# Kernel tuning notes

Hardware: AMD Instinct MI355X
Metric: run time of the kernel (lower is better)

The kernel has to match this reference:

```python
import jax, jax.numpy as jnp
import numpy as np

EPS = 1e-9  # Dice BatchNorm epsilon

def _dice(x, alpha, mm, mv):
    # Keras BN(center=False, scale=False) in inference mode: (x - moving_mean) / sqrt(moving_var + eps)
    p = jax.nn.sigmoid((x - mm) * jax.lax.rsqrt(mv + EPS))
    return x * (p + alpha * (1.0 - p))

def setup_inputs() -> dict:
    key = jax.random.key(0)
    ks = jax.random.split(key, 8)
    B, T, E = 4096, 200, 12
    return {
        "query": jax.random.normal(ks[0], (B, 1, E), jnp.float32),
        "keys": jax.random.normal(ks[1], (B, T, E), jnp.float32),
        "mask": jnp.ones((B, T), dtype=bool),
        "W0": jax.random.normal(ks[2], (48, 80), jnp.float32) * (1.0 / np.sqrt(48)),
        "b0": jnp.zeros((80,), jnp.float32),
        "W1": jax.random.normal(ks[3], (80, 40), jnp.float32) * (1.0 / np.sqrt(80)),
        "b1": jnp.zeros((40,), jnp.float32),
        "alpha0": jax.random.uniform(ks[4], (80,), jnp.float32),
        "alpha1": jax.random.uniform(ks[5], (40,), jnp.float32),
        "mm0": jnp.zeros((80,), jnp.float32),
        "mv0": jnp.ones((80,), jnp.float32),
        "mm1": jnp.zeros((40,), jnp.float32),
        "mv1": jnp.ones((40,), jnp.float32),
        "atten_kernel": jax.random.normal(ks[6], (40, 1), jnp.float32) * (1.0 / np.sqrt(40)),
        "atten_bias": jnp.zeros((1,), jnp.float32),
    }

def reference(query, keys, mask, W0, b0, W1, b1, alpha0, alpha1,
              mm0, mv0, mm1, mv1, atten_kernel, atten_bias):
    B, T, E = keys.shape
    q = jnp.broadcast_to(query, (B, T, E))  # K.repeat_elements(query, T, 1)
    att = jnp.concatenate([q, keys, q - keys, q * keys], axis=-1)  # [B, T, 4E=48]
    h = _dice(jnp.einsum('bti,io->bto', att, W0) + b0, alpha0, mm0, mv0)  # [B,T,80]
    h = _dice(jnp.einsum('bti,io->bto', h, W1) + b1, alpha1, mm1, mv1)    # [B,T,40]
    score = jnp.einsum('bti,io->bto', h, atten_kernel) + atten_bias       # [B,T,1]
    scores = jnp.swapaxes(score, 1, 2)  # [B,1,T]
    # NOTE: original code computes tf.where(mask,...) but overwrites it and
    # matmuls the UNMASKED scores with keys (bug reproduced faithfully).
    return jnp.matmul(scores, keys)  # [B,1,E]
```

## Files before the change

### kernel.cpp

```cpp
#include <hip/hip_runtime.h>
#include <math.h>

#define B_TOT 4096
#define T_LEN 200
#define E_DIM 12
#define LOG2E 1.44269504088896340736f

typedef __attribute__((ext_vector_type(8))) short     bf16x8;
typedef __attribute__((ext_vector_type(4))) float     f32x4;


__device__ inline unsigned short f2bf(float f) {
    union { float f; unsigned u; } x; x.f = f;
    unsigned r = x.u + 0x7FFFu + ((x.u >> 16) & 1u);
    return (unsigned short)(r >> 16);
}

__global__ __launch_bounds__(256) void din_prep(
    const float* __restrict__ W0, const float* __restrict__ b0v,
    const float* __restrict__ W1, const float* __restrict__ b1v,
    const float* __restrict__ a0, const float* __restrict__ a1,
    const float* __restrict__ mm0, const float* __restrict__ mv0,
    const float* __restrict__ mm1, const float* __restrict__ mv1,
    const float* __restrict__ ak, void* __restrict__ wsv)
{
    unsigned char* wsb = (unsigned char*)wsv;
    unsigned short* w0e = (unsigned short*)wsb;
    unsigned short* w1e = (unsigned short*)(wsb + 10240);
    float* d0c = (float*)(wsb + 19456);
    float* d1c = (float*)(wsb + 20736);

    int idx = blockIdx.x * 256 + threadIdx.x;
    if (idx < 5120) {
        int n = idx >> 6, k = idx & 63;
        float v;
        if (k < 12)        v = W0[(12 + k) * 80 + n] - W0[(24 + k) * 80 + n];
        else if (k < 24)   v = W0[(36 + (k - 12)) * 80 + n];
        else if (k < 36)   v = W0[(k - 24) * 80 + n] + W0[(24 + (k - 24)) * 80 + n];
        else if (k == 36)  v = b0v[n];
        else               v = 0.0f;
        w0e[n * 64 + k] = f2bf(v);
    } else if (idx < 9728) {
        int v2 = idx - 5120;
        int n = v2 / 96, k = v2 - n * 96;
        float v = 0.0f;
        if (n < 40) {
            if (k < 80)       v = W1[k * 40 + n];
            else if (k == 80) v = b1v[n];
        }
        w1e[n * 96 + k] = f2bf(v);
    } else if (idx < 10048) {
        int v2 = idx - 9728;
        int o = v2 >> 2, c = v2 & 3;
        float rs = rsqrtf(mv0[o] + 1e-9f) * LOG2E;
        float val = (c == 0) ? -rs : (c == 1) ? mm0[o] * rs : (c == 2) ? a0[o] : 1.0f - a0[o];
        d0c[o * 4 + c] = val;
    } else {
        int v2 = idx - 10048;
        int j = v2 >> 2, c = v2 & 3;
        float val = 0.0f;
        if (j < 40) {
            float rs = rsqrtf(mv1[j] + 1e-9f) * LOG2E;
            val = (c == 0) ? -rs : (c == 1) ? mm1[j] * rs : (c == 2) ? a1[j] * ak[j]
                                                          : (1.0f - a1[j]) * ak[j];
        }
        d1c[j * 4 + c] = val;
    }
}

#define A0_STRIDE 72
#define H_STRIDE  104

__global__ __launch_bounds__(256, 2) void din_mfma(
    const float* __restrict__ query, const float* __restrict__ keys,
    const float* __restrict__ abias_p, const void* __restrict__ wsv,
    float* __restrict__ out)
{
    __shared__ __align__(16) unsigned short A0[256 * A0_STRIDE];
    __shared__ __align__(16) unsigned short H[4 * 16 * H_STRIDE];
    __shared__ __align__(16) float SC[256];

    const unsigned char* wsb = (const unsigned char*)wsv;
    const unsigned short* w0e = (const unsigned short*)wsb;
    const unsigned short* w1e = (const unsigned short*)(wsb + 10240);
    const f32x4* d0cp = (const f32x4*)(wsb + 19456);
    const f32x4* d1cp = (const f32x4*)(wsb + 20736);

    const int tid = threadIdx.x;
    const int lane = tid & 63;
    const int w = tid >> 6;
    const int lane15 = lane & 15;
    const int quad = lane >> 4;

    const int p = blockIdx.x * 256 + tid;
    const int bq = p / T_LEN;

    float kk[12], qq[12];
    {
        const float4* kp = (const float4*)(keys + (size_t)p * E_DIM);
        float4 k0 = kp[0], k1 = kp[1], k2 = kp[2];
        kk[0]=k0.x; kk[1]=k0.y; kk[2]=k0.z; kk[3]=k0.w;
        kk[4]=k1.x; kk[5]=k1.y; kk[6]=k1.z; kk[7]=k1.w;
        kk[8]=k2.x; kk[9]=k2.y; kk[10]=k2.z; kk[11]=k2.w;
        const float4* qp = (const float4*)(query + (size_t)bq * E_DIM);
        float4 q0 = qp[0], q1 = qp[1], q2 = qp[2];
        qq[0]=q0.x; qq[1]=q0.y; qq[2]=q0.z; qq[3]=q0.w;
        qq[4]=q1.x; qq[5]=q1.y; qq[6]=q1.z; qq[7]=q1.w;
        qq[8]=q2.x; qq[9]=q2.y; qq[10]=q2.z; qq[11]=q2.w;
    }
    {
        unsigned short row[64];
        #pragma unroll
        for (int i = 0; i < 12; ++i) row[i]      = f2bf(kk[i]);
        #pragma unroll
        for (int i = 0; i < 12; ++i) row[12 + i] = f2bf(qq[i] * kk[i]);
        #pragma unroll
        for (int i = 0; i < 12; ++i) row[24 + i] = f2bf(qq[i]);
        row[36] = 0x3F80;
        #pragma unroll
        for (int i = 37; i < 64; ++i) row[i] = 0;
        unsigned short* dst = &A0[tid * A0_STRIDE];
        #pragma unroll
        for (int j = 0; j < 8; ++j) {
            bf16x8 v;
            #pragma unroll
            for (int c = 0; c < 8; ++c) v[c] = (short)row[j * 8 + c];
            *(bf16x8*)(dst + j * 8) = v;
        }
    }

    bf16x8 b0f[5][2];
    #pragma unroll
    for (int nt = 0; nt < 5; ++nt)
        #pragma unroll
        for (int ks = 0; ks < 2; ++ks)
            b0f[nt][ks] = *(const bf16x8*)(w0e + (nt * 16 + lane15) * 64 + ks * 32 + quad * 8);
    bf16x8 b1f[3][3];
    #pragma unroll
    for (int nt = 0; nt < 3; ++nt)
        #pragma unroll
        for (int ks = 0; ks < 3; ++ks)
            b1f[nt][ks] = *(const bf16x8*)(w1e + (nt * 16 + lane15) * 96 + ks * 32 + quad * 8);
    f32x4 d0c[5];
    #pragma unroll
    for (int nt = 0; nt < 5; ++nt) d0c[nt] = d0cp[nt * 16 + lane15];
    f32x4 d1c[3];
    #pragma unroll
    for (int nt = 0; nt < 3; ++nt) d1c[nt] = d1cp[nt * 16 + lane15];
    const float abias = abias_p[0];

    unsigned short* Hw = &H[w * 16 * H_STRIDE];
    if (quad == 0) {
        bf16x8 one8 = {(short)0x3F80, 0, 0, 0, 0, 0, 0, 0};
        bf16x8 zero8 = {0, 0, 0, 0, 0, 0, 0, 0};
        *(bf16x8*)(Hw + lane15 * H_STRIDE + 80) = one8;
        *(bf16x8*)(Hw + lane15 * H_STRIDE + 88) = zero8;
    }
    __syncthreads();

    #pragma unroll
    for (int ti = 0; ti < 4; ++ti) {
        const int tt = w * 4 + ti;
        const unsigned short* arow = &A0[(tt * 16 + lane15) * A0_STRIDE + quad * 8];
        bf16x8 a0 = *(const bf16x8*)arow;
        bf16x8 a1 = *(const bf16x8*)(arow + 32);

        f32x4 acc[5];
        #pragma unroll
        for (int nt = 0; nt < 5; ++nt) {
            f32x4 c = {0.f, 0.f, 0.f, 0.f};
            c = __builtin_amdgcn_mfma_f32_16x16x32_bf16(a0, b0f[nt][0], c, 0, 0, 0);
            c = __builtin_amdgcn_mfma_f32_16x16x32_bf16(a1, b0f[nt][1], c, 0, 0, 0);
            acc[nt] = c;
        }
        #pragma unroll
        for (int nt = 0; nt < 5; ++nt) {
            #pragma unroll
            for (int r = 0; r < 4; ++r) {
                float z = acc[nt][r];
                float pg = __builtin_amdgcn_rcpf(
                    1.0f + __builtin_amdgcn_exp2f(fmaf(z, d0c[nt].x, d0c[nt].y)));
                float h = z * fmaf(pg, d0c[nt].w, d0c[nt].z);
                Hw[(quad * 4 + r) * H_STRIDE + nt * 16 + lane15] = f2bf(h);
            }
        }
        __syncthreads();

        bf16x8 af[3];
        #pragma unroll
        for (int ks = 0; ks < 3; ++ks)
            af[ks] = *(const bf16x8*)(Hw + lane15 * H_STRIDE + ks * 32 + quad * 8);
        float s[4] = {0.f, 0.f, 0.f, 0.f};
        #pragma unroll
        for (int nt = 0; nt < 3; ++nt) {
            f32x4 c = {0.f, 0.f, 0.f, 0.f};
            #pragma unroll
            for (int ks = 0; ks < 3; ++ks)
                c = __builtin_amdgcn_mfma_f32_16x16x32_bf16(af[ks], b1f[nt][ks], c, 0, 0, 0);
            #pragma unroll
            for (int r = 0; r < 4; ++r) {
                float z = c[r];
                float pg = __builtin_amdgcn_rcpf(
                    1.0f + __builtin_amdgcn_exp2f(fmaf(z, d1c[nt].x, d1c[nt].y)));
                s[r] = fmaf(z, fmaf(pg, d1c[nt].w, d1c[nt].z), s[r]);
            }
        }
        #pragma unroll
        for (int m = 1; m < 16; m <<= 1) {
            #pragma unroll
            for (int r = 0; r < 4; ++r) s[r] += __shfl_xor(s[r], m, 64);
        }
        if (lane15 == 0) {
            float4 sv;
            sv.x = s[0] + abias; sv.y = s[1] + abias;
            sv.z = s[2] + abias; sv.w = s[3] + abias;
            *(float4*)&SC[tt * 16 + quad * 4] = sv;
        }
        __syncthreads();
    }

    float sc = SC[tid];
    float v[12];
    #pragma unroll
    for (int e = 0; e < 12; ++e) v[e] = sc * kk[e];
    int b0w = __shfl(bq, 0, 64);
    int b63 = __shfl(bq, 63, 64);
    float r0[12], r1[12];
    bool first = (bq == b0w);
    #pragma unroll
    for (int e = 0; e < 12; ++e) {
        r0[e] = first ? v[e] : 0.0f;
        r1[e] = first ? 0.0f : v[e];
    }
    #pragma unroll
    for (int m = 1; m < 64; m <<= 1) {
        #pragma unroll
        for (int e = 0; e < 12; ++e) {
            r0[e] += __shfl_xor(r0[e], m, 64);
            r1[e] += __shfl_xor(r1[e], m, 64);
        }
    }
    if (lane == 0) {
        #pragma unroll
        for (int e = 0; e < 12; ++e)
            atomicAdd(&out[(size_t)b0w * 12 + e], r0[e]);
        if (b63 != b0w) {
            #pragma unroll
            for (int e = 0; e < 12; ++e)
                atomicAdd(&out[(size_t)b63 * 12 + e], r1[e]);
        }
    }
}

extern "C" void kernel_launch(void* const* d_in, const int* in_sizes, int n_in,
                              void* d_out, int out_size, void* d_ws, size_t ws_size,
                              hipStream_t stream) {
    const float* query = (const float*)d_in[0];
    const float* keys  = (const float*)d_in[1];
    const float* W0  = (const float*)d_in[3];
    const float* b0v = (const float*)d_in[4];
    const float* W1  = (const float*)d_in[5];
    const float* b1v = (const float*)d_in[6];
    const float* a0  = (const float*)d_in[7];
    const float* a1  = (const float*)d_in[8];
    const float* mm0 = (const float*)d_in[9];
    const float* mv0 = (const float*)d_in[10];
    const float* mm1 = (const float*)d_in[11];
    const float* mv1 = (const float*)d_in[12];
    const float* ak  = (const float*)d_in[13];
    const float* ab  = (const float*)d_in[14];
    float* out = (float*)d_out;

    hipMemsetAsync(d_out, 0, (size_t)out_size * sizeof(float), stream);
    hipLaunchKernelGGL(din_prep, dim3(40), dim3(256), 0, stream,
                       W0, b0v, W1, b1v, a0, a1, mm0, mv0, mm1, mv1, ak, d_ws);
    hipLaunchKernelGGL(din_mfma, dim3(3200), dim3(256), 0, stream,
                       query, keys, ab, d_ws, out);
}
```

Before: 178.1 us.

## Assign one wavefront per batch row and reduce scores·keys with MFMA

Each wavefront now owns one batch row and walks its 200 timesteps in 64-row chunks, using wave-private LDS slices. This removes block-wide barriers, the cross-wave score staging and the atomics. The final scores·keys product is done with a bf16 MFMA over the bf16 keys already staged in LDS, so the output memset goes away and each row is written once. In exchange there are fewer, longer-running waves, with a partially wasted last chunk. The weighted sum of keys also drops from fp32 to bf16 inputs.

```diff
diff --git a/kernel.cpp b/kernel.cpp
--- a/kernel.cpp
+++ b/kernel.cpp
@@ -6,8 +6,8 @@
 #define E_DIM 12
 #define LOG2E 1.44269504088896340736f
 
-typedef __attribute__((ext_vector_type(8))) short     bf16x8;
-typedef __attribute__((ext_vector_type(4))) float     f32x4;
+typedef __attribute__((ext_vector_type(8))) short bf16x8;
+typedef __attribute__((ext_vector_type(4))) float f32x4;
 
 
 __device__ inline unsigned short f2bf(float f) {
@@ -76,9 +76,9 @@
     const float* __restrict__ abias_p, const void* __restrict__ wsv,
     float* __restrict__ out)
 {
-    __shared__ __align__(16) unsigned short A0[256 * A0_STRIDE];
+    __shared__ __align__(16) unsigned short Aseg[4 * 64];
+    __shared__ __align__(16) unsigned short A0[4 * 64 * A0_STRIDE];
     __shared__ __align__(16) unsigned short H[4 * 16 * H_STRIDE];
-    __shared__ __align__(16) float SC[256];
 
     const unsigned char* wsb = (const unsigned char*)wsv;
     const unsigned short* w0e = (const unsigned short*)wsb;
@@ -89,167 +89,175 @@
     const int tid = threadIdx.x;
     const int lane = tid & 63;
     const int w = tid >> 6;
-    const int lane15 = lane & 15;
+    const int l15 = lane & 15;
     const int quad = lane >> 4;
-
-    const int p = blockIdx.x * 256 + tid;
-    const int bq = p / T_LEN;
-
-    float kk[12], qq[12];
+    const int b = blockIdx.x * 4 + w;
+
+    unsigned short* A0w = &A0[w * 64 * A0_STRIDE];
+    unsigned short* Hw  = &H[w * 16 * H_STRIDE];
+    unsigned short* Asw = &Aseg[w * 64];
+
+    bf16x8 b0f[5][2];
+    #pragma unroll
+    for (int nt = 0; nt < 5; ++nt)
+        #pragma unroll
+        for (int ks = 0; ks < 2; ++ks)
+            b0f[nt][ks] = *(const bf16x8*)(w0e + (nt * 16 + l15) * 64 + ks * 32 + quad * 8);
+    bf16x8 b1f[3][3];
+    #pragma unroll
+    for (int nt = 0; nt < 3; ++nt)
+        #pragma unroll
+        for (int ks = 0; ks < 3; ++ks)
+            b1f[nt][ks] = *(const bf16x8*)(w1e + (nt * 16 + l15) * 96 + ks * 32 + quad * 8);
+    f32x4 d0c[5];
+    #pragma unroll
+    for (int nt = 0; nt < 5; ++nt) d0c[nt] = d0cp[nt * 16 + l15];
+    f32x4 d1c[3];
+    #pragma unroll
+    for (int nt = 0; nt < 3; ++nt) d1c[nt] = d1cp[nt * 16 + l15];
+    const float abias = abias_p[0];
+
+    float qq[12];
     {
-        const float4* kp = (const float4*)(keys + (size_t)p * E_DIM);
-        float4 k0 = kp[0], k1 = kp[1], k2 = kp[2];
-        kk[0]=k0.x; kk[1]=k0.y; kk[2]=k0.z; kk[3]=k0.w;
-        kk[4]=k1.x; kk[5]=k1.y; kk[6]=k1.z; kk[7]=k1.w;
-        kk[8]=k2.x; kk[9]=k2.y; kk[10]=k2.z; kk[11]=k2.w;
-        const float4* qp = (const float4*)(query + (size_t)bq * E_DIM);
+        const float4* qp = (const float4*)(query + (size_t)b * E_DIM);
         float4 q0 = qp[0], q1 = qp[1], q2 = qp[2];
         qq[0]=q0.x; qq[1]=q0.y; qq[2]=q0.z; qq[3]=q0.w;
         qq[4]=q1.x; qq[5]=q1.y; qq[6]=q1.z; qq[7]=q1.w;
         qq[8]=q2.x; qq[9]=q2.y; qq[10]=q2.z; qq[11]=q2.w;
     }
-    {
-        unsigned short row[64];
-        #pragma unroll
-        for (int i = 0; i < 12; ++i) row[i]      = f2bf(kk[i]);
-        #pragma unroll
-        for (int i = 0; i < 12; ++i) row[12 + i] = f2bf(qq[i] * kk[i]);
-        #pragma unroll
-        for (int i = 0; i < 12; ++i) row[24 + i] = f2bf(qq[i]);
-        row[36] = 0x3F80;
-        #pragma unroll
-        for (int i = 37; i < 64; ++i) row[i] = 0;
-        unsigned short* dst = &A0[tid * A0_STRIDE];
-        #pragma unroll
-        for (int j = 0; j < 8; ++j) {
-            bf16x8 v;
-            #pragma unroll
-            for (int c = 0; c < 8; ++c) v[c] = (short)row[j * 8 + c];
-            *(bf16x8*)(dst + j * 8) = v;
-        }
-    }
-
-    bf16x8 b0f[5][2];
-    #pragma unroll
-    for (int nt = 0; nt < 5; ++nt)
-        #pragma unroll
-        for (int ks = 0; ks < 2; ++ks)
-            b0f[nt][ks] = *(const bf16x8*)(w0e + (nt * 16 + lane15) * 64 + ks * 32 + quad * 8);
-    bf16x8 b1f[3][3];
-    #pragma unroll
-    for (int nt = 0; nt < 3; ++nt)
-        #pragma unroll
-        for (int ks = 0; ks < 3; ++ks)
-            b1f[nt][ks] = *(const bf16x8*)(w1e + (nt * 16 + lane15) * 96 + ks * 32 + quad * 8);
-    f32x4 d0c[5];
-    #pragma unroll
-    for (int nt = 0; nt < 5; ++nt) d0c[nt] = d0cp[nt * 16 + lane15];
-    f32x4 d1c[3];
-    #pragma unroll
-    for (int nt = 0; nt < 3; ++nt) d1c[nt] = d1cp[nt * 16 + lane15];
-    const float abias = abias_p[0];
-
-    unsigned short* Hw = &H[w * 16 * H_STRIDE];
+    unsigned qqw[6];
+    #pragma unroll
+    for (int i = 0; i < 6; ++i)
+        qqw[i] = (unsigned)f2bf(qq[2 * i]) | ((unsigned)f2bf(qq[2 * i + 1]) << 16);
+
     if (quad == 0) {
         bf16x8 one8 = {(short)0x3F80, 0, 0, 0, 0, 0, 0, 0};
         bf16x8 zero8 = {0, 0, 0, 0, 0, 0, 0, 0};
-        *(bf16x8*)(Hw + lane15 * H_STRIDE + 80) = one8;
-        *(bf16x8*)(Hw + lane15 * H_STRIDE + 88) = zero8;
-    }
-    __syncthreads();
-
-    #pragma unroll
-    for (int ti = 0; ti < 4; ++ti) {
-        const int tt = w * 4 + ti;
-        const unsigned short* arow = &A0[(tt * 16 + lane15) * A0_STRIDE + quad * 8];
-        bf16x8 a0 = *(const bf16x8*)arow;
-        bf16x8 a1 = *(const bf16x8*)(arow + 32);
-
-        f32x4 acc[5];
+        *(bf16x8*)(Hw + l15 * H_STRIDE + 80) = one8;
+        *(bf16x8*)(Hw + l15 * H_STRIDE + 88) = zero8;
+    }
+
+    f32x4 acc2 = {0.f, 0.f, 0.f, 0.f};
+
+    for (int c = 0; c < 4; ++c) {
+        const int t0 = c * 64;
+        const int myT = t0 + lane;
+        const bool valid = myT < T_LEN;
+
+        float kk[12];
+        if (valid) {
+            const float4* kp = (const float4*)(keys + ((size_t)b * T_LEN + myT) * E_DIM);
+            float4 k0 = kp[0], k1 = kp[1], k2 = kp[2];
+            kk[0]=k0.x; kk[1]=k0.y; kk[2]=k0.z; kk[3]=k0.w;
+            kk[4]=k1.x; kk[5]=k1.y; kk[6]=k1.z; kk[7]=k1.w;
+            kk[8]=k2.x; kk[9]=k2.y; kk[10]=k2.z; kk[11]=k2.w;
+        } else {
+            #pragma unroll
+            for (int i = 0; i < 12; ++i) kk[i] = 0.0f;
+        }
+        {
+            unsigned wds[32];
+            #pragma unroll
+            for (int i = 0; i < 6; ++i)
+                wds[i] = (unsigned)f2bf(kk[2 * i]) | ((unsigned)f2bf(kk[2 * i + 1]) << 16);
+            #pragma unroll
+            for (int i = 0; i < 6; ++i)
+                wds[6 + i] = (unsigned)f2bf(qq[2 * i] * kk[2 * i])
+                           | ((unsigned)f2bf(qq[2 * i + 1] * kk[2 * i + 1]) << 16);
+            #pragma unroll
+            for (int i = 0; i < 6; ++i) wds[12 + i] = qqw[i];
+            wds[18] = 0x00003F80u;
+            #pragma unroll
+            for (int i = 19; i < 32; ++i) wds[i] = 0u;
+            unsigned short* dst = A0w + lane * A0_STRIDE;
+            #pragma unroll
+            for (int v = 0; v < 8; ++v) {
+                bf16x8 pk;
+                #pragma unroll
+                for (int h = 0; h < 4; ++h) {
+                    unsigned u = wds[v * 4 + h];
+                    pk[2 * h]     = (short)(u & 0xFFFF);
+                    pk[2 * h + 1] = (short)(u >> 16);
+                }
+                *(bf16x8*)(dst + v * 8) = pk;
+            }
+        }
+        Asw[lane] = 0;
+
+        const int ntiles = (c < 3) ? 4 : 1;
+        for (int ti = 0; ti < ntiles; ++ti) {
+            const unsigned short* ar = A0w + (ti * 16 + l15) * A0_STRIDE + quad * 8;
+            bf16x8 a0 = *(const bf16x8*)ar;
+            bf16x8 a1 = *(const bf16x8*)(ar + 32);
+
+            f32x4 acc[5];
+            #pragma unroll
+            for (int nt = 0; nt < 5; ++nt) {
+                f32x4 cc = {0.f, 0.f, 0.f, 0.f};
+                cc = __builtin_amdgcn_mfma_f32_16x16x32_bf16(a0, b0f[nt][0], cc, 0, 0, 0);
+                cc = __builtin_amdgcn_mfma_f32_16x16x32_bf16(a1, b0f[nt][1], cc, 0, 0, 0);
+                acc[nt] = cc;
+            }
+            #pragma unroll
+            for (int nt = 0; nt < 5; ++nt) {
+                #pragma unroll
+                for (int r = 0; r < 4; ++r) {
+                    float z = acc[nt][r];
+                    float pg = __builtin_amdgcn_rcpf(
+                        1.0f + __builtin_amdgcn_exp2f(fmaf(z, d0c[nt].x, d0c[nt].y)));
+                    float h = z * fmaf(pg, d0c[nt].w, d0c[nt].z);
+                    Hw[(quad * 4 + r) * H_STRIDE + nt * 16 + l15] = f2bf(h);
+                }
+            }
+            bf16x8 af[3];
+            #pragma unroll
+            for (int ks = 0; ks < 3; ++ks)
+                af[ks] = *(const bf16x8*)(Hw + l15 * H_STRIDE + ks * 32 + quad * 8);
+            float s[4] = {0.f, 0.f, 0.f, 0.f};
+            #pragma unroll
+            for (int nt = 0; nt < 3; ++nt) {
+                f32x4 cc = {0.f, 0.f, 0.f, 0.f};
+                #pragma unroll
+                for (int ks = 0; ks < 3; ++ks)
+                    cc = __builtin_amdgcn_mfma_f32_16x16x32_bf16(af[ks], b1f[nt][ks], cc, 0, 0, 0);
+                #pragma unroll
+                for (int r = 0; r < 4; ++r) {
+                    float z = cc[r];
+                    float pg = __builtin_amdgcn_rcpf(
+                        1.0f + __builtin_amdgcn_exp2f(fmaf(z, d1c[nt].x, d1c[nt].y)));
+                    s[r] = fmaf(z, fmaf(pg, d1c[nt].w, d1c[nt].z), s[r]);
+                }
+            }
+            #pragma unroll
+            for (int m = 1; m < 16; m <<= 1) {
+                #pragma unroll
+                for (int r = 0; r < 4; ++r) s[r] += __shfl_xor(s[r], m, 64);
+            }
+            if (l15 == 0) {
+                unsigned long long pk = 0ull;
+                #pragma unroll
+                for (int r = 0; r < 4; ++r) {
+                    int t = t0 + ti * 16 + quad * 4 + r;
+                    unsigned short sb = (t < T_LEN) ? f2bf(s[r] + abias) : (unsigned short)0;
+                    pk |= (unsigned long long)sb << (16 * r);
+                }
+                *(unsigned long long*)(Asw + ti * 16 + quad * 4) = pk;
+            }
+        }
+
         #pragma unroll
-        for (int nt = 0; nt < 5; ++nt) {
-            f32x4 c = {0.f, 0.f, 0.f, 0.f};
-            c = __builtin_amdgcn_mfma_f32_16x16x32_bf16(a0, b0f[nt][0], c, 0, 0, 0);
-            c = __builtin_amdgcn_mfma_f32_16x16x32_bf16(a1, b0f[nt][1], c, 0, 0, 0);
-            acc[nt] = c;
-        }
-        #pragma unroll
-        for (int nt = 0; nt < 5; ++nt) {
-            #pragma unroll
-            for (int r = 0; r < 4; ++r) {
-                float z = acc[nt][r];
-                float pg = __builtin_amdgcn_rcpf(
-                    1.0f + __builtin_amdgcn_exp2f(fmaf(z, d0c[nt].x, d0c[nt].y)));
-                float h = z * fmaf(pg, d0c[nt].w, d0c[nt].z);
-                Hw[(quad * 4 + r) * H_STRIDE + nt * 16 + lane15] = f2bf(h);
-            }
-        }
-        __syncthreads();
-
-        bf16x8 af[3];
-        #pragma unroll
-        for (int ks = 0; ks < 3; ++ks)
-            af[ks] = *(const bf16x8*)(Hw + lane15 * H_STRIDE + ks * 32 + quad * 8);
-        float s[4] = {0.f, 0.f, 0.f, 0.f};
-        #pragma unroll
-        for (int nt = 0; nt < 3; ++nt) {
-            f32x4 c = {0.f, 0.f, 0.f, 0.f};
-            #pragma unroll
-            for (int ks = 0; ks < 3; ++ks)
-                c = __builtin_amdgcn_mfma_f32_16x16x32_bf16(af[ks], b1f[nt][ks], c, 0, 0, 0);
-            #pragma unroll
-            for (int r = 0; r < 4; ++r) {
-                float z = c[r];
-                float pg = __builtin_amdgcn_rcpf(
-                    1.0f + __builtin_amdgcn_exp2f(fmaf(z, d1c[nt].x, d1c[nt].y)));
-                s[r] = fmaf(z, fmaf(pg, d1c[nt].w, d1c[nt].z), s[r]);
-            }
-        }
-        #pragma unroll
-        for (int m = 1; m < 16; m <<= 1) {
-            #pragma unroll
-            for (int r = 0; r < 4; ++r) s[r] += __shfl_xor(s[r], m, 64);
-        }
-        if (lane15 == 0) {
-            float4 sv;
-            sv.x = s[0] + abias; sv.y = s[1] + abias;
-            sv.z = s[2] + abias; sv.w = s[3] + abias;
-            *(float4*)&SC[tt * 16 + quad * 4] = sv;
-        }
-        __syncthreads();
-    }
-
-    float sc = SC[tid];
-    float v[12];
-    #pragma unroll
-    for (int e = 0; e < 12; ++e) v[e] = sc * kk[e];
-    int b0w = __shfl(bq, 0, 64);
-    int b63 = __shfl(bq, 63, 64);
-    float r0[12], r1[12];
-    bool first = (bq == b0w);
-    #pragma unroll
-    for (int e = 0; e < 12; ++e) {
-        r0[e] = first ? v[e] : 0.0f;
-        r1[e] = first ? 0.0f : v[e];
-    }
-    #pragma unroll
-    for (int m = 1; m < 64; m <<= 1) {
-        #pragma unroll
-        for (int e = 0; e < 12; ++e) {
-            r0[e] += __shfl_xor(r0[e], m, 64);
-            r1[e] += __shfl_xor(r1[e], m, 64);
-        }
-    }
-    if (lane == 0) {
-        #pragma unroll
-        for (int e = 0; e < 12; ++e)
-            atomicAdd(&out[(size_t)b0w * 12 + e], r0[e]);
-        if (b63 != b0w) {
-            #pragma unroll
-            for (int e = 0; e < 12; ++e)
-                atomicAdd(&out[(size_t)b63 * 12 + e], r1[e]);
-        }
-    }
+        for (int ks = 0; ks < 2; ++ks) {
+            bf16x8 pa = *(const bf16x8*)(Asw + l15 * 64 + ks * 32 + quad * 8);
+            bf16x8 bk;
+            #pragma unroll
+            for (int j = 0; j < 8; ++j)
+                bk[j] = (short)A0w[(ks * 32 + quad * 8 + j) * A0_STRIDE + l15];
+            acc2 = __builtin_amdgcn_mfma_f32_16x16x32_bf16(pa, bk, acc2, 0, 0, 0);
+        }
+    }
+
+    if (quad == 0 && l15 < 12)
+        out[(size_t)b * E_DIM + l15] = acc2[0];
 }
 
 extern "C" void kernel_launch(void* const* d_in, const int* in_sizes, int n_in,
@@ -271,9 +279,8 @@
     const float* ab  = (const float*)d_in[14];
     float* out = (float*)d_out;
 
-    hipMemsetAsync(d_out, 0, (size_t)out_size * sizeof(float), stream);
     hipLaunchKernelGGL(din_prep, dim3(40), dim3(256), 0, stream,
                        W0, b0v, W1, b1v, a0, a1, mm0, mv0, mm1, mv1, ak, d_ws);
-    hipLaunchKernelGGL(din_mfma, dim3(3200), dim3(256), 0, stream,
+    hipLaunchKernelGGL(din_mfma, dim3(B_TOT / 4), dim3(256), 0, stream,
                        query, keys, ab, d_ws, out);
 }
```

Result: faster. 155.9 us (-12.5%).
